# Kernel tuning notes

Measured on AMD Instinct MI355X. Metric: run time of the kernel, lower is better.

The kernel has to match this reference:

```python
import jax, jax.numpy as jnp
import numpy as np

H = 16        # num_attention_heads
HS = 128      # head_size
ROT = 32      # rotary_ndims (partial RoPE, NeoX rotary_pct=0.25)
BASE = 10000.0


def _rope_cache(seq_len):
    inv_freq = 1.0 / (BASE ** (jnp.arange(0, ROT, 2, dtype=jnp.float32) / ROT))
    t = jnp.arange(seq_len, dtype=jnp.float32)
    freqs = jnp.outer(t, inv_freq)                      # [s, ROT/2]
    emb = jnp.concatenate([freqs, freqs], axis=-1)      # [s, ROT]
    return jnp.cos(emb), jnp.sin(emb)


def _rotate_half(x):
    x1, x2 = jnp.split(x, 2, axis=-1)
    return jnp.concatenate([-x2, x1], axis=-1)


def setup_inputs() -> dict:
    key = jax.random.key(0)
    k1, k2, k3 = jax.random.split(key, 3)
    B, S, D = 2, 2048, 2048
    hidden_states = jax.random.normal(k1, (B, S, D), dtype=jnp.float32)
    position_ids = jnp.broadcast_to(jnp.arange(S, dtype=jnp.int64 if jax.config.jax_enable_x64 else jnp.int32), (B, S))
    W_qkv = jax.random.normal(k2, (D, 3 * H * HS), dtype=jnp.float32) * 0.02
    b_qkv = jnp.zeros((3 * H * HS,), dtype=jnp.float32)
    W_dense = jax.random.normal(k3, (H * HS, D), dtype=jnp.float32) * 0.02
    b_dense = jnp.zeros((D,), dtype=jnp.float32)
    return {"hidden_states": hidden_states, "position_ids": position_ids,
            "W_qkv": W_qkv, "b_qkv": b_qkv, "W_dense": W_dense, "b_dense": b_dense}


def reference(hidden_states, position_ids, W_qkv, b_qkv, W_dense, b_dense):
    B, S, D = hidden_states.shape
    # fused QKV projection, NeoX layout: [b, s, h, 3*hs]
    qkv = (hidden_states @ W_qkv + b_qkv).reshape(B, S, H, 3 * HS)
    q = qkv[..., :HS]            # [b, s, h, hs]
    k = qkv[..., HS:2 * HS]
    v = qkv[..., 2 * HS:]

    # partial rotary embedding on first ROT dims
    cos, sin = _rope_cache(S)                       # [s, ROT]
    cos = cos[position_ids][:, :, None, :]          # [b, s, 1, ROT]
    sin = sin[position_ids][:, :, None, :]
    q_rot, q_pass = q[..., :ROT], q[..., ROT:]
    k_rot, k_pass = k[..., :ROT], k[..., ROT:]
    q_rot = q_rot * cos + _rotate_half(q_rot) * sin
    k_rot = k_rot * cos + _rotate_half(k_rot) * sin
    q = jnp.concatenate([q_rot, q_pass], axis=-1)
    k = jnp.concatenate([k_rot, k_pass], axis=-1)

    # scaled dot-product attention (no mask, as in the source SDPA call)
    scale = 1.0 / jnp.sqrt(jnp.asarray(HS, dtype=q.dtype))
    scores = jnp.einsum('bqhd,bkhd->bhqk', q, k) * scale   # [b, h, s, s]
    attn = jax.nn.softmax(scores, axis=-1)
    out = jnp.einsum('bhqk,bkhd->bqhd', attn, v)            # [b, s, h, hs]
    out = out.reshape(B, S, H * HS)                         # 'b h d n -> b d (h n)'
    return out @ W_dense + b_dense
```

## Files before the change

kernel.cpp:

```cpp
#include <hip/hip_runtime.h>

typedef short bf16x8 __attribute__((ext_vector_type(8)));
typedef float f32x4 __attribute__((ext_vector_type(4)));

#define S_LEN 2048
#define NHEAD 16
#define HSZ 128

__device__ __forceinline__ float bf2f(ushort u) {
    union { unsigned int i; float f; } x; x.i = ((unsigned int)u) << 16; return x.f;
}
__device__ __forceinline__ ushort f2bf(float f) {
    union { float f; unsigned int i; } x; x.f = f;
    unsigned int r = (x.i + 0x7FFFu + ((x.i >> 16) & 1u)) >> 16;
    return (ushort)r;
}

__device__ __forceinline__ void gload16(const ushort* g, ushort* l) {
    __builtin_amdgcn_global_load_lds(
        (const __attribute__((address_space(1))) unsigned int*)g,
        (__attribute__((address_space(3))) unsigned int*)l,
        16, 0, 0);
}

__global__ void cast_kernel(const float* __restrict__ in, ushort* __restrict__ out, int n4) {
    int i = blockIdx.x * 256 + threadIdx.x;
    if (i >= n4) return;
    float4 v = ((const float4*)in)[i];
    ushort4 r;
    r.x = f2bf(v.x); r.y = f2bf(v.y); r.z = f2bf(v.z); r.w = f2bf(v.w);
    ((ushort4*)out)[i] = r;
}

__global__ void transpose_cast(const float* __restrict__ W, ushort* __restrict__ WT,
                               int K, int N) {
    __shared__ float tile[32][33];
    int n = blockIdx.x * 32 + threadIdx.x;
    #pragma unroll
    for (int j = 0; j < 32; j += 8) {
        int k = blockIdx.y * 32 + threadIdx.y + j;
        tile[threadIdx.y + j][threadIdx.x] = W[(size_t)k * N + n];
    }
    __syncthreads();
    int k2 = blockIdx.y * 32 + threadIdx.x;
    #pragma unroll
    for (int j = 0; j < 32; j += 8) {
        int n2 = blockIdx.x * 32 + threadIdx.y + j;
        WT[(size_t)n2 * K + k2] = f2bf(tile[threadIdx.x][threadIdx.y + j]);
    }
}

template <int EPI>
__global__ __launch_bounds__(256) void gemm128(
    const ushort* __restrict__ A, const ushort* __restrict__ Bt,
    const float* __restrict__ bias, float* __restrict__ Cout, int Kdim, int Ndim,
    ushort* __restrict__ q_out, ushort* __restrict__ k_out, ushort* __restrict__ v_out) {
    __shared__ __align__(16) ushort lA[2][128 * 32];
    __shared__ __align__(16) ushort lB[2][128 * 32];
    const int tid = threadIdx.x;
    const int m0 = blockIdx.y * 128, n0 = blockIdx.x * 128;
    const int lane = tid & 63, wid = tid >> 6;
    const int wm = wid >> 1, wn = wid & 1, lm = lane & 15, quad = lane >> 4;
    const int srow = tid >> 2;
    const int gc = (tid & 3) ^ ((tid >> 3) & 3);
    const int wb8 = (wid << 6) * 8;
    const int cs = (quad ^ ((lm >> 1) & 3)) * 8;

    const ushort* pA = A  + (size_t)(m0 + srow) * Kdim + gc * 8;
    const ushort* pB = Bt + (size_t)(n0 + srow) * Kdim + gc * 8;
    const size_t rhalf = (size_t)64 * Kdim;

    const int fA = (wm * 64 + lm) * 32;
    const int fB = (wn * 64 + lm) * 32;

    f32x4 acc[16];
    #pragma unroll
    for (int i = 0; i < 16; ++i) acc[i] = (f32x4){0.f, 0.f, 0.f, 0.f};

    const int T = Kdim >> 5;
    gload16(pA,         lA[0] + wb8);
    gload16(pA + rhalf, lA[0] + 2048 + wb8);
    gload16(pB,         lB[0] + wb8);
    gload16(pB + rhalf, lB[0] + 2048 + wb8);
    pA += 32; pB += 32;

    for (int t = 0; t < T; ++t) {
        __syncthreads();
        const ushort* la = lA[t & 1];
        const ushort* lb = lB[t & 1];
        if (t + 1 < T) {
            ushort* da = lA[(t + 1) & 1];
            ushort* db = lB[(t + 1) & 1];
            gload16(pA,         da + wb8);
            gload16(pA + rhalf, da + 2048 + wb8);
            gload16(pB,         db + wb8);
            gload16(pB + rhalf, db + 2048 + wb8);
            pA += 32; pB += 32;
        }
        bf16x8 af[4], bfr[4];
        #pragma unroll
        for (int t4 = 0; t4 < 4; ++t4) {
            af[t4]  = *(const bf16x8*)(la + fA + t4 * 512 + cs);
            bfr[t4] = *(const bf16x8*)(lb + fB + t4 * 512 + cs);
        }
        #pragma unroll
        for (int mt = 0; mt < 4; ++mt)
            #pragma unroll
            for (int nt = 0; nt < 4; ++nt)
                acc[mt * 4 + nt] = __builtin_amdgcn_mfma_f32_16x16x32_bf16(
                    af[mt], bfr[nt], acc[mt * 4 + nt], 0, 0, 0);
    }

    #pragma unroll
    for (int mt = 0; mt < 4; ++mt) {
        #pragma unroll
        for (int nt = 0; nt < 4; ++nt) {
            f32x4 c = acc[mt * 4 + nt];
            int gn = n0 + wn * 64 + nt * 16 + lm;
            float bv = bias[gn];
            #pragma unroll
            for (int i = 0; i < 4; ++i) {
                int gm = m0 + wm * 64 + mt * 16 + quad * 4 + i;
                float v = c[i] + bv;
                if (EPI == 0) {
                    int h = gn / 384, r = gn - h * 384;
                    int t = r >> 7, d = r & 127;
                    int b = gm >> 11, s = gm & 2047;
                    ushort bb = f2bf(v);
                    if (t == 0) {
                        q_out[((size_t)(b * NHEAD + h) * S_LEN + s) * HSZ + d] = bb;
                    } else if (t == 1) {
                        k_out[((size_t)(b * NHEAD + h) * S_LEN + s) * HSZ + d] = bb;
                    } else {
                        v_out[((size_t)(b * NHEAD + h) * HSZ + d) * S_LEN + s] = bb;
                    }
                } else {
                    Cout[(size_t)gm * Ndim + gn] = v;
                }
            }
        }
    }
}

__global__ void rope_kernel(ushort* __restrict__ Qr, ushort* __restrict__ Kr,
                            const int* __restrict__ pos_ids) {
    int idx = blockIdx.x * 256 + threadIdx.x;
    int j = idx & 15;
    int row = idx >> 4;
    int s = row & 2047;
    int bh = row >> 11;
    int b = bh >> 4;
    int pos = pos_ids[b * S_LEN + s];
    double inv = exp2(-(double)j * (13.287712379549449 / 16.0));
    double th = (double)pos * inv;
    float c = (float)cos(th), sn = (float)sin(th);
    size_t base = (size_t)row * HSZ;
    {
        float x1 = bf2f(Qr[base + j]), x2 = bf2f(Qr[base + j + 16]);
        Qr[base + j]      = f2bf(x1 * c - x2 * sn);
        Qr[base + j + 16] = f2bf(x2 * c + x1 * sn);
    }
    {
        float x1 = bf2f(Kr[base + j]), x2 = bf2f(Kr[base + j + 16]);
        Kr[base + j]      = f2bf(x1 * c - x2 * sn);
        Kr[base + j + 16] = f2bf(x2 * c + x1 * sn);
    }
}

__global__ __launch_bounds__(256, 2) void attn_mfma(
    const ushort* __restrict__ Q, const ushort* __restrict__ K,
    const ushort* __restrict__ Vt, ushort* __restrict__ O) {
    __shared__ __align__(16) ushort lQ[128 * 136];
    __shared__ __align__(16) ushort lK[2][32 * 128];
    __shared__ __align__(16) ushort lVt[2][128 * 32];
    __shared__ __align__(16) ushort lP[4 * 32 * 40];

    const int tid = threadIdx.x;
    const int wid = tid >> 6, lane = tid & 63;
    const int L = lane & 15, quad = lane >> 4;
    const int bh = blockIdx.y;
    const int q0 = blockIdx.x * 128;
    const int wq0 = wid * 32;
    const size_t base = (size_t)bh * S_LEN * HSZ;
    const ushort* Qb = Q + base + (size_t)q0 * HSZ;
    const ushort* Kb = K + base;
    const ushort* Vb = Vt + base;
    ushort* lPw = lP + wid * (32 * 40);

    #pragma unroll
    for (int p = 0; p < 8; ++p) {
        int idx = tid + p * 256;
        int row = idx >> 4, ch = idx & 15;
        uint4 v = ((const uint4*)Qb)[idx];
        *(uint4*)(lQ + row * 136 + ch * 8) = v;
    }
    __syncthreads();

    bf16x8 qf[2][4];
    #pragma unroll
    for (int qs = 0; qs < 2; ++qs)
        #pragma unroll
        for (int dc = 0; dc < 4; ++dc)
            qf[qs][dc] = *(const bf16x8*)(lQ + (wq0 + qs * 16 + L) * 136 + dc * 32 + quad * 8);

    int kx[4];
    #pragma unroll
    for (int dc = 0; dc < 4; ++dc) kx[dc] = (((dc * 4 + quad) ^ (L & 7))) * 8;
    const int vx = (quad ^ ((L >> 1) & 3)) * 8;

    const int li0 = tid, li1 = tid + 256;
    const int ub0 = ((tid & 192)) * 8, ub1 = ((tid & 192) + 256) * 8;
    const int kr0 = li0 >> 4, kg0 = (li0 & 15) ^ (kr0 & 7);
    const int kr1 = li1 >> 4, kg1 = (li1 & 15) ^ (kr1 & 7);
    const int vd0 = li0 >> 2, vg0 = (li0 & 3) ^ ((vd0 >> 1) & 3);
    const int vd1 = li1 >> 2, vg1 = (li1 & 3) ^ ((vd1 >> 1) & 3);

    f32x4 acc_o[8][2];
    #pragma unroll
    for (int dt = 0; dt < 8; ++dt)
        #pragma unroll
        for (int qs = 0; qs < 2; ++qs) acc_o[dt][qs] = (f32x4){0.f, 0.f, 0.f, 0.f};
    float lacc[2] = {0.f, 0.f};
    const float scale = 0.08838834764831845f;
    const float SHIFT = 12.0f;

    {
        gload16(Kb + (size_t)kr0 * 128 + kg0 * 8, lK[0] + ub0);
        gload16(Kb + (size_t)kr1 * 128 + kg1 * 8, lK[0] + ub1);
        gload16(Vb + (size_t)vd0 * 2048 + vg0 * 8, lVt[0] + ub0);
        gload16(Vb + (size_t)vd1 * 2048 + vg1 * 8, lVt[0] + ub1);
    }

    for (int kt = 0; kt < S_LEN / 32; ++kt) {
        __syncthreads();
        const int cur = kt & 1;
        const ushort* lKc = lK[cur];
        const ushort* lVc = lVt[cur];
        if (kt + 1 < S_LEN / 32) {
            ushort* dK = lK[cur ^ 1];
            ushort* dV = lVt[cur ^ 1];
            int kb = (kt + 1) * 32;
            gload16(Kb + (size_t)(kb + kr0) * 128 + kg0 * 8, dK + ub0);
            gload16(Kb + (size_t)(kb + kr1) * 128 + kg1 * 8, dK + ub1);
            gload16(Vb + (size_t)vd0 * 2048 + kb + vg0 * 8, dV + ub0);
            gload16(Vb + (size_t)vd1 * 2048 + kb + vg1 * 8, dV + ub1);
        }

        f32x4 sa[2][2];
        #pragma unroll
        for (int t = 0; t < 2; ++t)
            #pragma unroll
            for (int qs = 0; qs < 2; ++qs) sa[t][qs] = (f32x4){0.f, 0.f, 0.f, 0.f};
        #pragma unroll
        for (int t = 0; t < 2; ++t)
            #pragma unroll
            for (int dc = 0; dc < 4; ++dc) {
                bf16x8 kf = *(const bf16x8*)(lKc + (t * 16 + L) * 128 + kx[dc]);
                sa[t][0] = __builtin_amdgcn_mfma_f32_16x16x32_bf16(kf, qf[0][dc], sa[t][0], 0, 0, 0);
                sa[t][1] = __builtin_amdgcn_mfma_f32_16x16x32_bf16(kf, qf[1][dc], sa[t][1], 0, 0, 0);
            }

        #pragma unroll
        for (int t = 0; t < 2; ++t)
            #pragma unroll
            for (int qs = 0; qs < 2; ++qs) {
                #pragma unroll
                for (int r = 0; r < 4; ++r) {
                    float pv = __expf(fmaf(sa[t][qs][r], scale, -SHIFT));
                    lacc[qs] += pv;
                    sa[t][qs][r] = pv;
                }
                ushort4 u;
                u.x = f2bf(sa[t][qs][0]);
                u.y = f2bf(sa[t][qs][1]);
                u.z = f2bf(sa[t][qs][2]);
                u.w = f2bf(sa[t][qs][3]);
                *(ushort4*)(lPw + (qs * 16 + L) * 40 + t * 16 + quad * 4) = u;
            }
        __asm__ volatile("s_waitcnt lgkmcnt(0)" ::: "memory");

        bf16x8 pf0 = *(const bf16x8*)(lPw + L * 40 + quad * 8);
        bf16x8 pf1 = *(const bf16x8*)(lPw + (16 + L) * 40 + quad * 8);
        #pragma unroll
        for (int dt = 0; dt < 8; ++dt) {
            bf16x8 vf = *(const bf16x8*)(lVc + (dt * 16 + L) * 32 + vx);
            acc_o[dt][0] = __builtin_amdgcn_mfma_f32_16x16x32_bf16(vf, pf0, acc_o[dt][0], 0, 0, 0);
            acc_o[dt][1] = __builtin_amdgcn_mfma_f32_16x16x32_bf16(vf, pf1, acc_o[dt][1], 0, 0, 0);
        }
    }

    const int b = bh >> 4, h = bh & 15;
    #pragma unroll
    for (int qs = 0; qs < 2; ++qs) {
        float l = lacc[qs];
        l += __shfl_xor(l, 16);
        l += __shfl_xor(l, 32);
        float inv = 1.f / l;
        size_t row = ((size_t)(b * S_LEN + q0 + wq0 + qs * 16 + L)) * (NHEAD * HSZ) + h * HSZ;
        #pragma unroll
        for (int dt = 0; dt < 8; ++dt) {
            ushort4 u;
            u.x = f2bf(acc_o[dt][qs][0] * inv);
            u.y = f2bf(acc_o[dt][qs][1] * inv);
            u.z = f2bf(acc_o[dt][qs][2] * inv);
            u.w = f2bf(acc_o[dt][qs][3] * inv);
            *(ushort4*)(O + row + dt * 16 + quad * 4) = u;
        }
    }
}

extern "C" void kernel_launch(void* const* d_in, const int* in_sizes, int n_in,
                              void* d_out, int out_size, void* d_ws, size_t ws_size,
                              hipStream_t stream) {
    const float* hidden = (const float*)d_in[0];
    const int*   pos    = (const int*)d_in[1];
    const float* Wqkv   = (const float*)d_in[2];
    const float* bqkv   = (const float*)d_in[3];
    const float* Wd     = (const float*)d_in[4];
    const float* bd     = (const float*)d_in[5];

    char* ws = (char*)d_ws;
    ushort* hA  = (ushort*)ws;
    ushort* WqT = (ushort*)(ws + 16777216ull);
    ushort* WdT = (ushort*)(ws + 41943040ull);
    ushort* Qb  = (ushort*)(ws + 50331648ull);
    ushort* Kb  = (ushort*)(ws + 67108864ull);
    ushort* Vb  = (ushort*)(ws + 83886080ull);

    cast_kernel<<<dim3(8192), dim3(256), 0, stream>>>(hidden, hA, 2097152);
    transpose_cast<<<dim3(192, 64), dim3(32, 8), 0, stream>>>(Wqkv, WqT, 2048, 6144);
    transpose_cast<<<dim3(64, 64), dim3(32, 8), 0, stream>>>(Wd, WdT, 2048, 2048);

    gemm128<0><<<dim3(48, 32), dim3(256), 0, stream>>>(hA, WqT, bqkv, nullptr, 2048, 6144,
                                                       Qb, Kb, Vb);
    rope_kernel<<<dim3(4096), dim3(256), 0, stream>>>(Qb, Kb, pos);

    ushort* Obuf = hA;
    attn_mfma<<<dim3(16, 32), dim3(256), 0, stream>>>(Qb, Kb, Vb, Obuf);

    gemm128<1><<<dim3(16, 32), dim3(256), 0, stream>>>(Obuf, WdT, bd, (float*)d_out,
                                                       2048, 2048, nullptr, nullptr, nullptr);
}
```

Baseline: 440.8 us.

## Use 256x256 tiled GEMM for QKV projection and float sincos in RoPE

Adds a 512-thread GEMM kernel with 256x256 output tiles and a 4-stage LDS ring buffer, loading two k-steps ahead and splitting the MFMA work into two halves interleaved with the global-to-LDS loads. It replaces the 128x128 GEMM for the QKV projection to get more operand reuse per LDS load and better latency hiding. The RoPE kernel also switches from double-precision exp2/cos/sin to float exp2f and sincosf, which is cheaper but may drift slightly in accuracy at large positions. The larger tile gives only 384 blocks and needs a lot of LDS and registers per block, which could limit occupancy.

Result: no change. 442.3 us (+0.4%).

```diff
diff --git a/kernel.cpp b/kernel.cpp
--- a/kernel.cpp
+++ b/kernel.cpp
@@ -47,6 +47,125 @@
     for (int j = 0; j < 32; j += 8) {
         int n2 = blockIdx.x * 32 + threadIdx.y + j;
         WT[(size_t)n2 * K + k2] = f2bf(tile[threadIdx.x][threadIdx.y + j]);
+    }
+}
+
+template <int EPI>
+__global__ __launch_bounds__(512, 2) void gemm256(
+    const ushort* __restrict__ A, const ushort* __restrict__ Bt,
+    const float* __restrict__ bias, float* __restrict__ Cout, int Kdim, int Ndim,
+    ushort* __restrict__ q_out, ushort* __restrict__ k_out, ushort* __restrict__ v_out) {
+    __shared__ __align__(16) ushort lA[4][8192];
+    __shared__ __align__(16) ushort lB[4][8192];
+    const int tid = threadIdx.x;
+    const int m0 = blockIdx.y * 256, n0 = blockIdx.x * 256;
+    const int lane = tid & 63, wid = tid >> 6;
+    const int wm = wid >> 2, wn = wid & 3;
+    const int lm = lane & 15, quad = lane >> 4;
+    const int srow = tid >> 2;
+    const int g8 = ((tid & 3) ^ ((tid >> 3) & 3)) * 8;
+    const int wb = wid * 512;
+    const int ch8 = (quad ^ ((lm >> 1) & 3)) * 8;
+    const int aoff = (wm * 128 + lm) * 32 + ch8;
+    const int boff = (wn * 64 + lm) * 32 + ch8;
+
+    const ushort* pA = A + (size_t)(m0 + srow) * Kdim + g8;
+    const ushort* pB = Bt + (size_t)(n0 + srow) * Kdim + g8;
+    const size_t rhalf = (size_t)128 * Kdim;
+
+    f32x4 acc[8][4];
+    #pragma unroll
+    for (int i = 0; i < 8; ++i)
+        #pragma unroll
+        for (int j = 0; j < 4; ++j) acc[i][j] = (f32x4){0.f, 0.f, 0.f, 0.f};
+
+    const int T = Kdim >> 5;
+    gload16(pA,              lA[0] + wb);
+    gload16(pA + rhalf,      lA[0] + 4096 + wb);
+    gload16(pB,              lB[0] + wb);
+    gload16(pB + rhalf,      lB[0] + 4096 + wb);
+    gload16(pA + 32,         lA[1] + wb);
+    gload16(pA + 32 + rhalf, lA[1] + 4096 + wb);
+    gload16(pB + 32,         lB[1] + wb);
+    gload16(pB + 32 + rhalf, lB[1] + 4096 + wb);
+    asm volatile("s_waitcnt vmcnt(4)" ::: "memory");
+    asm volatile("s_barrier" ::: "memory");
+
+    for (int t = 0; t < T; ++t) {
+        const ushort* la = lA[t & 3];
+        const ushort* lb = lB[t & 3];
+        bf16x8 af[4], bfr[4];
+        #pragma unroll
+        for (int mt = 0; mt < 4; ++mt) af[mt] = *(const bf16x8*)(la + aoff + mt * 512);
+        #pragma unroll
+        for (int nt = 0; nt < 4; ++nt) bfr[nt] = *(const bf16x8*)(lb + boff + nt * 512);
+        if (t + 2 < T) {
+            ushort* da = lA[(t + 2) & 3];
+            const ushort* sa = pA + (size_t)(t + 2) * 32;
+            gload16(sa,         da + wb);
+            gload16(sa + rhalf, da + 4096 + wb);
+        }
+        asm volatile("s_barrier" ::: "memory");
+        __builtin_amdgcn_s_setprio(1);
+        #pragma unroll
+        for (int mt = 0; mt < 4; ++mt)
+            #pragma unroll
+            for (int nt = 0; nt < 4; ++nt)
+                acc[mt][nt] = __builtin_amdgcn_mfma_f32_16x16x32_bf16(
+                    af[mt], bfr[nt], acc[mt][nt], 0, 0, 0);
+        __builtin_amdgcn_s_setprio(0);
+
+        bf16x8 af2[4];
+        #pragma unroll
+        for (int mt = 0; mt < 4; ++mt) af2[mt] = *(const bf16x8*)(la + aoff + 2048 + mt * 512);
+        if (t + 2 < T) {
+            ushort* db = lB[(t + 2) & 3];
+            const ushort* sb = pB + (size_t)(t + 2) * 32;
+            gload16(sb,         db + wb);
+            gload16(sb + rhalf, db + 4096 + wb);
+        }
+        asm volatile("s_barrier" ::: "memory");
+        __builtin_amdgcn_s_setprio(1);
+        #pragma unroll
+        for (int mt = 0; mt < 4; ++mt)
+            #pragma unroll
+            for (int nt = 0; nt < 4; ++nt)
+                acc[4 + mt][nt] = __builtin_amdgcn_mfma_f32_16x16x32_bf16(
+                    af2[mt], bfr[nt], acc[4 + mt][nt], 0, 0, 0);
+        __builtin_amdgcn_s_setprio(0);
+        if (t + 2 < T) asm volatile("s_waitcnt vmcnt(4)" ::: "memory");
+        else           asm volatile("s_waitcnt vmcnt(0)" ::: "memory");
+        asm volatile("s_barrier" ::: "memory");
+    }
+
+    #pragma unroll
+    for (int mt = 0; mt < 8; ++mt) {
+        #pragma unroll
+        for (int nt = 0; nt < 4; ++nt) {
+            f32x4 c = acc[mt][nt];
+            int gn = n0 + wn * 64 + nt * 16 + lm;
+            float bv = bias[gn];
+            #pragma unroll
+            for (int i = 0; i < 4; ++i) {
+                int gm = m0 + wm * 128 + mt * 16 + quad * 4 + i;
+                float v = c[i] + bv;
+                if (EPI == 0) {
+                    int h = gn / 384, r = gn - h * 384;
+                    int tt = r >> 7, d = r & 127;
+                    int b = gm >> 11, s = gm & 2047;
+                    ushort bb = f2bf(v);
+                    if (tt == 0) {
+                        q_out[((size_t)(b * NHEAD + h) * S_LEN + s) * HSZ + d] = bb;
+                    } else if (tt == 1) {
+                        k_out[((size_t)(b * NHEAD + h) * S_LEN + s) * HSZ + d] = bb;
+                    } else {
+                        v_out[((size_t)(b * NHEAD + h) * HSZ + d) * S_LEN + s] = bb;
+                    }
+                } else {
+                    Cout[(size_t)gm * Ndim + gn] = v;
+                }
+            }
+        }
     }
 }
 
@@ -151,9 +270,10 @@
     int bh = row >> 11;
     int b = bh >> 4;
     int pos = pos_ids[b * S_LEN + s];
-    double inv = exp2(-(double)j * (13.287712379549449 / 16.0));
-    double th = (double)pos * inv;
-    float c = (float)cos(th), sn = (float)sin(th);
+    float inv = exp2f((float)j * -0.8304820237218405f);
+    float th = (float)pos * inv;
+    float sn, c;
+    sincosf(th, &sn, &c);
     size_t base = (size_t)row * HSZ;
     {
         float x1 = bf2f(Qr[base + j]), x2 = bf2f(Qr[base + j + 16]);
@@ -331,7 +451,7 @@
     transpose_cast<<<dim3(192, 64), dim3(32, 8), 0, stream>>>(Wqkv, WqT, 2048, 6144);
     transpose_cast<<<dim3(64, 64), dim3(32, 8), 0, stream>>>(Wd, WdT, 2048, 2048);
 
-    gemm128<0><<<dim3(48, 32), dim3(256), 0, stream>>>(hA, WqT, bqkv, nullptr, 2048, 6144,
+    gemm256<0><<<dim3(24, 16), dim3(512), 0, stream>>>(hA, WqT, bqkv, nullptr, 2048, 6144,
                                                        Qb, Kb, Vb);
     rope_kernel<<<dim3(4096), dim3(256), 0, stream>>>(Qb, Kb, pos);
 
```
